# Kernel tuning notes

Measured on AMD Instinct MI355X. Metric: run time of the kernel, lower is better.

## Reference

```python
import jax, jax.numpy as jnp
import numpy as np

D_IN, H1, H2, F1 = 2048, 128, 64, 32


def setup_inputs() -> dict:
    key = jax.random.key(0)
    ks = jax.random.split(key, 13)
    s = lambda *sh: 1.0 / np.sqrt(sh[-1])
    return {
        "x": jax.random.normal(ks[0], (64, 512, D_IN), dtype=jnp.float32),
        "W_ih1": jax.random.uniform(ks[1], (H1, D_IN), jnp.float32, -s(H1), s(H1)),
        "W_hh1": jax.random.uniform(ks[2], (H1, H1), jnp.float32, -s(H1), s(H1)),
        "b_ih1": jax.random.uniform(ks[3], (H1,), jnp.float32, -s(H1), s(H1)),
        "b_hh1": jax.random.uniform(ks[4], (H1,), jnp.float32, -s(H1), s(H1)),
        "W_ih2": jax.random.uniform(ks[5], (H2, H1), jnp.float32, -s(H2), s(H2)),
        "W_hh2": jax.random.uniform(ks[6], (H2, H2), jnp.float32, -s(H2), s(H2)),
        "b_ih2": jax.random.uniform(ks[7], (H2,), jnp.float32, -s(H2), s(H2)),
        "b_hh2": jax.random.uniform(ks[8], (H2,), jnp.float32, -s(H2), s(H2)),
        "W_fc1": jax.random.uniform(ks[9], (F1, H2), jnp.float32, -s(F1), s(F1)),
        "b_fc1": jax.random.uniform(ks[10], (F1,), jnp.float32, -s(F1), s(F1)),
        "W_fc2": jax.random.uniform(ks[11], (1, F1), jnp.float32, -s(1), s(1)),
        "b_fc2": jax.random.uniform(ks[12], (1,), jnp.float32, -s(1), s(1)),
    }


def _rnn(x, W_ih, W_hh, b_ih, b_hh):
    # x: [B, T, D] -> outputs [B, T, H] (tanh RNN, h0 = 0)
    B = x.shape[0]
    H = W_hh.shape[0]
    # precompute the input projection once (big GEMM, outside the scan)
    xp = jnp.einsum('btd,hd->bth', x, W_ih) + b_ih  # [B, T, H]
    xp_t = jnp.swapaxes(xp, 0, 1)  # [T, B, H]

    def step(h, xpt):
        h_new = jnp.tanh(xpt + h @ W_hh.T + b_hh)
        return h_new, h_new

    h0 = jnp.zeros((B, H), dtype=x.dtype)
    _, ys = jax.lax.scan(step, h0, xp_t)  # ys: [T, B, H]
    return jnp.swapaxes(ys, 0, 1)


def reference(x, W_ih1, W_hh1, b_ih1, b_hh1, W_ih2, W_hh2, b_ih2, b_hh2,
              W_fc1, b_fc1, W_fc2, b_fc2):
    out1 = _rnn(x, W_ih1, W_hh1, b_ih1, b_hh1)      # [B, T, 128]
    # dropout is identity in eval mode
    out2 = _rnn(out1, W_ih2, W_hh2, b_ih2, b_hh2)   # [B, T, 64]
    h_last = out2[:, -1, :]                          # [B, 64]
    h = jax.nn.relu(h_last @ W_fc1.T + b_fc1)        # [B, 32]
    return h @ W_fc2.T + b_fc2                       # [B, 1]
```

## Files before the change

kernel.cpp:

```cpp
#include <hip/hip_runtime.h>

#define TT   512
#define DIN  2048
#define NH1  128
#define NH2  64
#define NB   64

typedef __attribute__((ext_vector_type(8))) __bf16 bf16x8;
typedef __attribute__((ext_vector_type(4))) float f32x4;
typedef __attribute__((ext_vector_type(2))) float f32x2;

__device__ __forceinline__ float tanh_fast(float x) {
    x = fminf(fmaxf(x, -15.0f), 15.0f);
    float e = __expf(2.0f * x);
    return (e - 1.0f) / (e + 1.0f);
}

__device__ __forceinline__ float rlane(float v, int l) {
    return __int_as_float(__builtin_amdgcn_readlane(__float_as_int(v), l));
}

__device__ __forceinline__ void pkfma(f32x2& acc, f32x2 w, f32x2 h) {
    asm("v_pk_fma_f32 %0, %1, %2, %0" : "+v"(acc) : "v"(w), "v"(h));
}

#define BAR() asm volatile("s_waitcnt lgkmcnt(0)\n\ts_barrier" ::: "memory")

__global__ __launch_bounds__(256, 1) void xp1_gemm(const float* __restrict__ x,
                                                   const float* __restrict__ W,
                                                   const float* __restrict__ bih1,
                                                   const float* __restrict__ bhh1,
                                                   float* __restrict__ xp1) {
    __shared__ __align__(16) __bf16 wl[2][NH1][40];

    const int tid  = threadIdx.x;
    const int lane = tid & 63;
    const int wv   = tid >> 6;
    const int quad = lane >> 4;
    const int l16  = lane & 15;
    const int m0   = blockIdx.x * 128 + wv * 32;

    const int wr = tid >> 1;
    const int wk = (tid & 1) * 16;

    float bias[8];
#pragma unroll
    for (int nt = 0; nt < 8; ++nt)
        bias[nt] = bih1[nt * 16 + l16] + bhh1[nt * 16 + l16];

    f32x4 acc[2][8];
#pragma unroll
    for (int ms = 0; ms < 2; ++ms)
#pragma unroll
        for (int nt = 0; nt < 8; ++nt)
            acc[ms][nt] = (f32x4){0.f, 0.f, 0.f, 0.f};

    const float* xr0 = x + (size_t)(m0 + l16) * DIN + quad * 8;
    const float* xr1 = x + (size_t)(m0 + 16 + l16) * DIN + quad * 8;
    const float* wp  = W + (size_t)wr * DIN + wk;

    float4 xa0 = *(const float4*)(xr0);
    float4 xb0 = *(const float4*)(xr0 + 4);
    float4 xa1 = *(const float4*)(xr1);
    float4 xb1 = *(const float4*)(xr1 + 4);
    float4 w0  = *(const float4*)(wp);
    float4 w1  = *(const float4*)(wp + 4);
    float4 w2  = *(const float4*)(wp + 8);
    float4 w3  = *(const float4*)(wp + 12);

    for (int kc = 0; kc < DIN; kc += 32) {
        {
            float wf[16] = {w0.x, w0.y, w0.z, w0.w, w1.x, w1.y, w1.z, w1.w,
                            w2.x, w2.y, w2.z, w2.w, w3.x, w3.y, w3.z, w3.w};
            bf16x8 hv0, lv0, hv1, lv1;
#pragma unroll
            for (int j = 0; j < 8; ++j) {
                __bf16 h = (__bf16)wf[j];
                hv0[j] = h;
                lv0[j] = (__bf16)(wf[j] - (float)h);
            }
#pragma unroll
            for (int j = 0; j < 8; ++j) {
                __bf16 h = (__bf16)wf[8 + j];
                hv1[j] = h;
                lv1[j] = (__bf16)(wf[8 + j] - (float)h);
            }
            *(bf16x8*)&wl[0][wr][wk]     = hv0;
            *(bf16x8*)&wl[0][wr][wk + 8] = hv1;
            *(bf16x8*)&wl[1][wr][wk]     = lv0;
            *(bf16x8*)&wl[1][wr][wk + 8] = lv1;
        }
        BAR();

        bf16x8 ah0, al0, ah1, al1;
        {
            float f0[8] = {xa0.x, xa0.y, xa0.z, xa0.w, xb0.x, xb0.y, xb0.z, xb0.w};
            float f1[8] = {xa1.x, xa1.y, xa1.z, xa1.w, xb1.x, xb1.y, xb1.z, xb1.w};
#pragma unroll
            for (int j = 0; j < 8; ++j) {
                __bf16 h0 = (__bf16)f0[j];
                ah0[j] = h0;
                al0[j] = (__bf16)(f0[j] - (float)h0);
                __bf16 h1 = (__bf16)f1[j];
                ah1[j] = h1;
                al1[j] = (__bf16)(f1[j] - (float)h1);
            }
        }

        if (kc + 32 < DIN) {
            xa0 = *(const float4*)(xr0 + kc + 32);
            xb0 = *(const float4*)(xr0 + kc + 36);
            xa1 = *(const float4*)(xr1 + kc + 32);
            xb1 = *(const float4*)(xr1 + kc + 36);
            w0  = *(const float4*)(wp + kc + 32);
            w1  = *(const float4*)(wp + kc + 36);
            w2  = *(const float4*)(wp + kc + 40);
            w3  = *(const float4*)(wp + kc + 44);
        }

#pragma unroll
        for (int nt = 0; nt < 8; ++nt) {
            bf16x8 bh = *(bf16x8*)&wl[0][nt * 16 + l16][quad * 8];
            bf16x8 bl = *(bf16x8*)&wl[1][nt * 16 + l16][quad * 8];
            acc[0][nt] = __builtin_amdgcn_mfma_f32_16x16x32_bf16(ah0, bh, acc[0][nt], 0, 0, 0);
            acc[0][nt] = __builtin_amdgcn_mfma_f32_16x16x32_bf16(al0, bh, acc[0][nt], 0, 0, 0);
            acc[0][nt] = __builtin_amdgcn_mfma_f32_16x16x32_bf16(ah0, bl, acc[0][nt], 0, 0, 0);
            acc[1][nt] = __builtin_amdgcn_mfma_f32_16x16x32_bf16(ah1, bh, acc[1][nt], 0, 0, 0);
            acc[1][nt] = __builtin_amdgcn_mfma_f32_16x16x32_bf16(al1, bh, acc[1][nt], 0, 0, 0);
            acc[1][nt] = __builtin_amdgcn_mfma_f32_16x16x32_bf16(ah1, bl, acc[1][nt], 0, 0, 0);
        }
        BAR();
    }

#pragma unroll
    for (int ms = 0; ms < 2; ++ms) {
        const int mb = m0 + ms * 16 + quad * 4;
#pragma unroll
        for (int nt = 0; nt < 8; ++nt) {
#pragma unroll
            for (int r = 0; r < 4; ++r)
                xp1[(size_t)(mb + r) * NH1 + nt * 16 + l16] = acc[ms][nt][r] + bias[nt];
        }
    }
}

__global__ __launch_bounds__(256, 1) void rnn_scan(
        const float* __restrict__ xp1,  const float* __restrict__ Whh1,
        const float* __restrict__ Wih2, const float* __restrict__ Whh2,
        const float* __restrict__ bih2, const float* __restrict__ bhh2,
        const float* __restrict__ Wfc1, const float* __restrict__ bfc1,
        const float* __restrict__ Wfc2, const float* __restrict__ bfc2,
        float* __restrict__ out) {
    __shared__ __align__(16) float h1buf[2][NH1];
    __shared__ __align__(16) float xp2buf[2][NH2];
    __shared__ __align__(16) float h2buf[2][NH2];

    const int tid  = threadIdx.x;
    const int lane = tid & 63;
    const int wv   = tid >> 6;
    const int b    = blockIdx.x;

    f32x2 w2[64];
    float b2 = 0.0f;

    if (wv <= 1) {
        const int row = wv * 64 + lane;
        const float4* src = (const float4*)(Whh1 + (size_t)row * NH1);
#pragma unroll
        for (int i = 0; i < 32; ++i) {
            float4 v = src[i];
            w2[2 * i]     = (f32x2){v.x, v.y};
            w2[2 * i + 1] = (f32x2){v.z, v.w};
        }
    } else if (wv == 2) {
        const float4* src = (const float4*)(Wih2 + (size_t)lane * NH1);
#pragma unroll
        for (int i = 0; i < 32; ++i) {
            float4 v = src[i];
            w2[2 * i]     = (f32x2){v.x, v.y};
            w2[2 * i + 1] = (f32x2){v.z, v.w};
        }
        b2 = bih2[lane] + bhh2[lane];
    } else {
        const float4* src = (const float4*)(Whh2 + (size_t)lane * NH2);
#pragma unroll
        for (int i = 0; i < 16; ++i) {
            float4 v = src[i];
            w2[2 * i]     = (f32x2){v.x, v.y};
            w2[2 * i + 1] = (f32x2){v.z, v.w};
        }
    }

    if (tid < 128) h1buf[0][tid] = 0.0f;
    if (tid < 64)  { h2buf[0][tid] = 0.0f; h2buf[1][tid] = 0.0f; }

    const int row = wv * 64 + lane;
    const float* xprow = xp1 + ((size_t)b * TT) * NH1 + row;

    float xr[8], xrn[8];
    if (wv <= 1) {
#pragma unroll
        for (int j = 0; j < 8; ++j) xr[j] = xprow[(size_t)j * NH1];
    }

    __syncthreads();

    for (int g = 0; g < 64; ++g) {
        if (wv <= 1 && g < 63) {
            const size_t t0 = (size_t)(g + 1) * 8;
#pragma unroll
            for (int j = 0; j < 8; ++j) xrn[j] = xprow[(t0 + j) * NH1];
        }
#pragma unroll
        for (int j = 0; j < 8; ++j) {
            const int s   = 8 * g + j + 1;
            const int cur = j & 1;
            const int nxt = cur ^ 1;
            if (wv <= 1) {
                f32x2 aA = (f32x2){xr[j], 0.0f};
                f32x2 aB = (f32x2){0.0f, 0.0f};
#pragma unroll
                for (int i = 0; i < 32; ++i) {
                    float4 h4 = *(const float4*)&h1buf[cur][4 * i];
                    pkfma(aA, w2[2 * i],     (f32x2){h4.x, h4.y});
                    pkfma(aB, w2[2 * i + 1], (f32x2){h4.z, h4.w});
                }
                float hv = tanh_fast((aA.x + aA.y) + (aB.x + aB.y));
                h1buf[nxt][row] = hv;
            } else if (wv == 2) {
                if (s >= 2) {
                    f32x2 aA = (f32x2){b2, 0.0f};
                    f32x2 aB = (f32x2){0.0f, 0.0f};
#pragma unroll
                    for (int i = 0; i < 32; ++i) {
                        float4 h4 = *(const float4*)&h1buf[cur][4 * i];
                        pkfma(aA, w2[2 * i],     (f32x2){h4.x, h4.y});
                        pkfma(aB, w2[2 * i + 1], (f32x2){h4.z, h4.w});
                    }
                    xp2buf[j & 1][lane] = (aA.x + aA.y) + (aB.x + aB.y);
                }
            } else {
                if (s >= 3) {
                    float xv = xp2buf[(j + 1) & 1][lane];
                    f32x2 aA = (f32x2){0.0f, 0.0f};
                    f32x2 aB = (f32x2){0.0f, 0.0f};
#pragma unroll
                    for (int i = 0; i < 16; ++i) {
                        float4 h4 = *(const float4*)&h2buf[cur][4 * i];
                        pkfma(aA, w2[2 * i],     (f32x2){h4.x, h4.y});
                        pkfma(aB, w2[2 * i + 1], (f32x2){h4.z, h4.w});
                    }
                    float h2v = tanh_fast(xv + ((aA.x + aA.y) + (aB.x + aB.y)));
                    h2buf[nxt][lane] = h2v;
                }
            }
            BAR();
        }
        if (wv <= 1 && g < 63) {
#pragma unroll
            for (int j = 0; j < 8; ++j) xr[j] = xrn[j];
        }
    }

    {
        if (wv == 2) {
            f32x2 aA = (f32x2){b2, 0.0f};
            f32x2 aB = (f32x2){0.0f, 0.0f};
#pragma unroll
            for (int i = 0; i < 32; ++i) {
                float4 h4 = *(const float4*)&h1buf[0][4 * i];
                pkfma(aA, w2[2 * i],     (f32x2){h4.x, h4.y});
                pkfma(aB, w2[2 * i + 1], (f32x2){h4.z, h4.w});
            }
            xp2buf[0][lane] = (aA.x + aA.y) + (aB.x + aB.y);
        } else if (wv == 3) {
            float xv = xp2buf[1][lane];
            f32x2 aA = (f32x2){0.0f, 0.0f};
            f32x2 aB = (f32x2){0.0f, 0.0f};
#pragma unroll
            for (int i = 0; i < 16; ++i) {
                float4 h4 = *(const float4*)&h2buf[0][4 * i];
                pkfma(aA, w2[2 * i],     (f32x2){h4.x, h4.y});
                pkfma(aB, w2[2 * i + 1], (f32x2){h4.z, h4.w});
            }
            float h2v = tanh_fast(xv + ((aA.x + aA.y) + (aB.x + aB.y)));
            h2buf[1][lane] = h2v;
        }
        BAR();
    }
    if (wv == 3) {
        float xv = xp2buf[0][lane];
        f32x2 aA = (f32x2){0.0f, 0.0f};
        f32x2 aB = (f32x2){0.0f, 0.0f};
#pragma unroll
        for (int i = 0; i < 16; ++i) {
            float4 h4 = *(const float4*)&h2buf[1][4 * i];
            pkfma(aA, w2[2 * i],     (f32x2){h4.x, h4.y});
            pkfma(aB, w2[2 * i + 1], (f32x2){h4.z, h4.w});
        }
        float h2last = tanh_fast(xv + ((aA.x + aA.y) + (aB.x + aB.y)));

        float wfc[64];
        const int fr = lane & 31;
        const float4* fsrc = (const float4*)(Wfc1 + (size_t)fr * NH2);
#pragma unroll
        for (int i = 0; i < 16; ++i) {
            float4 v = fsrc[i];
            wfc[4*i+0] = v.x; wfc[4*i+1] = v.y;
            wfc[4*i+2] = v.z; wfc[4*i+3] = v.w;
        }
        float a = (lane < 32) ? bfc1[lane] : 0.0f;
#pragma unroll
        for (int k = 0; k < 64; ++k)
            a = fmaf(wfc[k], rlane(h2last, k), a);
        float v = (lane < 32) ? fmaxf(a, 0.0f) * Wfc2[lane] : 0.0f;
#pragma unroll
        for (int off = 16; off > 0; off >>= 1) v += __shfl_down(v, off);
        if (lane == 0) out[b] = v + bfc2[0];
    }
}

extern "C" void kernel_launch(void* const* d_in, const int* in_sizes, int n_in,
                              void* d_out, int out_size, void* d_ws, size_t ws_size,
                              hipStream_t stream) {
    const float* x     = (const float*)d_in[0];
    const float* Wih1  = (const float*)d_in[1];
    const float* Whh1  = (const float*)d_in[2];
    const float* bih1  = (const float*)d_in[3];
    const float* bhh1  = (const float*)d_in[4];
    const float* Wih2  = (const float*)d_in[5];
    const float* Whh2  = (const float*)d_in[6];
    const float* bih2  = (const float*)d_in[7];
    const float* bhh2  = (const float*)d_in[8];
    const float* Wfc1  = (const float*)d_in[9];
    const float* bfc1  = (const float*)d_in[10];
    const float* Wfc2  = (const float*)d_in[11];
    const float* bfc2  = (const float*)d_in[12];
    float* outp = (float*)d_out;

    float* xp1 = (float*)d_ws;

    xp1_gemm<<<dim3((NB * TT) / 128), dim3(256), 0, stream>>>(x, Wih1, bih1, bhh1, xp1);
    rnn_scan<<<dim3(NB), dim3(256), 0, stream>>>(xp1, Whh1, Wih2, Whh2, bih2, bhh2,
                                                 Wfc1, bfc1, Wfc2, bfc2, outp);
}
```

Before: 717.0 us.

## Batch 16 sequences per block and run recurrence on MFMA with split-bf16

The recurrent scan now processes 16 sequences per workgroup and computes the hidden-state matvecs as 16x16x32 bf16 MFMAs. Weights and hidden states are split into hi/lo bf16 pairs, and three MFMAs per tile approximate fp32 precision. Hidden states live in XOR-swizzled LDS buffers. All four waves now share layer-1, the layer-2 input projection and the layer-2 recurrence instead of having dedicated roles. This reduces the grid from 64 blocks to 4, trading parallelism across CUs for more work per serial step, and the split-bf16 scheme carries some precision risk.

```diff
diff --git a/kernel.cpp b/kernel.cpp
--- a/kernel.cpp
+++ b/kernel.cpp
@@ -7,21 +7,13 @@
 #define NB   64
 
 typedef __attribute__((ext_vector_type(8))) __bf16 bf16x8;
+typedef __attribute__((ext_vector_type(4))) __bf16 bf16x4;
 typedef __attribute__((ext_vector_type(4))) float f32x4;
-typedef __attribute__((ext_vector_type(2))) float f32x2;
 
 __device__ __forceinline__ float tanh_fast(float x) {
     x = fminf(fmaxf(x, -15.0f), 15.0f);
     float e = __expf(2.0f * x);
     return (e - 1.0f) / (e + 1.0f);
-}
-
-__device__ __forceinline__ float rlane(float v, int l) {
-    return __int_as_float(__builtin_amdgcn_readlane(__float_as_int(v), l));
-}
-
-__device__ __forceinline__ void pkfma(f32x2& acc, f32x2 w, f32x2 h) {
-    asm("v_pk_fma_f32 %0, %1, %2, %0" : "+v"(acc) : "v"(w), "v"(h));
 }
 
 #define BAR() asm volatile("s_waitcnt lgkmcnt(0)\n\ts_barrier" ::: "memory")
@@ -144,6 +136,118 @@
     }
 }
 
+
+__device__ __forceinline__ f32x4 mfma3(bf16x8 ah, bf16x8 al, bf16x8 bh, bf16x8 bl, f32x4 c) {
+    c = __builtin_amdgcn_mfma_f32_16x16x32_bf16(ah, bh, c, 0, 0, 0);
+    c = __builtin_amdgcn_mfma_f32_16x16x32_bf16(al, bh, c, 0, 0, 0);
+    c = __builtin_amdgcn_mfma_f32_16x16x32_bf16(ah, bl, c, 0, 0, 0);
+    return c;
+}
+
+__device__ __forceinline__ void tanh_split4(const f32x4& a, bf16x4& hv, bf16x4& lv) {
+#pragma unroll
+    for (int r = 0; r < 4; ++r) {
+        float t = tanh_fast(a[r]);
+        __bf16 h = (__bf16)t;
+        hv[r] = h;
+        lv[r] = (__bf16)(t - (float)h);
+    }
+}
+
+__device__ __forceinline__ void load_split8(const float* p, bf16x8& hv, bf16x8& lv) {
+    float4 u = *(const float4*)p;
+    float4 v = *(const float4*)(p + 4);
+    float f[8] = {u.x, u.y, u.z, u.w, v.x, v.y, v.z, v.w};
+#pragma unroll
+    for (int j = 0; j < 8; ++j) {
+        __bf16 h = (__bf16)f[j];
+        hv[j] = h;
+        lv[j] = (__bf16)(f[j] - (float)h);
+    }
+}
+
+template <int CUR>
+__device__ __forceinline__ void scan_step(
+        int s, int wv, int q, int l16, int sw, int s0,
+        const float* __restrict__ xp1,
+        __bf16 (&h1hi)[2][16][NH1], __bf16 (&h1lo)[2][16][NH1],
+        __bf16 (&h2hi)[2][16][NH2], __bf16 (&h2lo)[2][16][NH2],
+        const bf16x8 (&a1h)[2][4], const bf16x8 (&a1l)[2][4],
+        const bf16x8 (&a2h)[4],    const bf16x8 (&a2l)[4],
+        const bf16x8 (&a3h)[2],    const bf16x8 (&a3l)[2],
+        const f32x4& b2f, f32x4& xpPrev, f32x4& x0, f32x4& x1) {
+    const int NXT = CUR ^ 1;
+
+    bf16x8 bh1[4], bl1[4];
+    {
+        const char* rbh = (const char*)&h1hi[CUR][l16][0];
+        const char* rbl = (const char*)&h1lo[CUR][l16][0];
+#pragma unroll
+        for (int kt = 0; kt < 4; ++kt) {
+            const int boff = (kt * 64 + q * 16) ^ sw;
+            bh1[kt] = *(const bf16x8*)(rbh + boff);
+            bl1[kt] = *(const bf16x8*)(rbl + boff);
+        }
+    }
+
+    f32x4 acc0 = x0;
+    f32x4 acc1 = x1;
+#pragma unroll
+    for (int kt = 0; kt < 4; ++kt)
+        acc0 = mfma3(a1h[0][kt], a1l[0][kt], bh1[kt], bl1[kt], acc0);
+#pragma unroll
+    for (int kt = 0; kt < 4; ++kt)
+        acc1 = mfma3(a1h[1][kt], a1l[1][kt], bh1[kt], bl1[kt], acc1);
+
+    bf16x4 hv0, lv0, hv1, lv1;
+    tanh_split4(acc0, hv0, lv0);
+    tanh_split4(acc1, hv1, lv1);
+    {
+        char* wbh = (char*)&h1hi[NXT][l16][0];
+        char* wbl = (char*)&h1lo[NXT][l16][0];
+        const int w0 = ((wv * 32 + q * 4) * 2) ^ sw;
+        const int w1 = ((wv * 32 + 16 + q * 4) * 2) ^ sw;
+        *(bf16x4*)(wbh + w0) = hv0;
+        *(bf16x4*)(wbl + w0) = lv0;
+        *(bf16x4*)(wbh + w1) = hv1;
+        *(bf16x4*)(wbl + w1) = lv1;
+    }
+
+    if (s + 2 <= TT) {
+        const float* p = xp1 + ((size_t)(s0 + l16) * TT + (s + 1)) * NH1 + wv * 32 + q * 4;
+        x0 = *(const f32x4*)p;
+        x1 = *(const f32x4*)(p + 16);
+    }
+
+    f32x4 x2 = b2f;
+#pragma unroll
+    for (int kt = 0; kt < 4; ++kt)
+        x2 = mfma3(a2h[kt], a2l[kt], bh1[kt], bl1[kt], x2);
+
+    if (s >= 3) {
+        bf16x8 bh2[2], bl2[2];
+        const char* r2h = (const char*)&h2hi[CUR][l16][0];
+        const char* r2l = (const char*)&h2lo[CUR][l16][0];
+#pragma unroll
+        for (int kt = 0; kt < 2; ++kt) {
+            const int boff = (kt * 64 + q * 16) ^ sw;
+            bh2[kt] = *(const bf16x8*)(r2h + boff);
+            bl2[kt] = *(const bf16x8*)(r2l + boff);
+        }
+        f32x4 a2 = xpPrev;
+#pragma unroll
+        for (int kt = 0; kt < 2; ++kt)
+            a2 = mfma3(a3h[kt], a3l[kt], bh2[kt], bl2[kt], a2);
+        bf16x4 hv2, lv2;
+        tanh_split4(a2, hv2, lv2);
+        const int w2o = ((wv * 16 + q * 4) * 2) ^ sw;
+        *(bf16x4*)((char*)&h2hi[NXT][l16][0] + w2o) = hv2;
+        *(bf16x4*)((char*)&h2lo[NXT][l16][0] + w2o) = lv2;
+    }
+    xpPrev = x2;
+    BAR();
+}
+
 __global__ __launch_bounds__(256, 1) void rnn_scan(
         const float* __restrict__ xp1,  const float* __restrict__ Whh1,
         const float* __restrict__ Wih2, const float* __restrict__ Whh2,
@@ -151,172 +255,165 @@
         const float* __restrict__ Wfc1, const float* __restrict__ bfc1,
         const float* __restrict__ Wfc2, const float* __restrict__ bfc2,
         float* __restrict__ out) {
-    __shared__ __align__(16) float h1buf[2][NH1];
-    __shared__ __align__(16) float xp2buf[2][NH2];
-    __shared__ __align__(16) float h2buf[2][NH2];
+    __shared__ __align__(16) __bf16 h1hi[2][16][NH1];
+    __shared__ __align__(16) __bf16 h1lo[2][16][NH1];
+    __shared__ __align__(16) __bf16 h2hi[2][16][NH2];
+    __shared__ __align__(16) __bf16 h2lo[2][16][NH2];
+    __shared__ __align__(16) float  h2fin[16][NH2];
 
     const int tid  = threadIdx.x;
     const int lane = tid & 63;
     const int wv   = tid >> 6;
-    const int b    = blockIdx.x;
-
-    f32x2 w2[64];
-    float b2 = 0.0f;
-
-    if (wv <= 1) {
-        const int row = wv * 64 + lane;
-        const float4* src = (const float4*)(Whh1 + (size_t)row * NH1);
-#pragma unroll
-        for (int i = 0; i < 32; ++i) {
-            float4 v = src[i];
-            w2[2 * i]     = (f32x2){v.x, v.y};
-            w2[2 * i + 1] = (f32x2){v.z, v.w};
-        }
-    } else if (wv == 2) {
-        const float4* src = (const float4*)(Wih2 + (size_t)lane * NH1);
-#pragma unroll
-        for (int i = 0; i < 32; ++i) {
-            float4 v = src[i];
-            w2[2 * i]     = (f32x2){v.x, v.y};
-            w2[2 * i + 1] = (f32x2){v.z, v.w};
-        }
-        b2 = bih2[lane] + bhh2[lane];
-    } else {
-        const float4* src = (const float4*)(Whh2 + (size_t)lane * NH2);
-#pragma unroll
-        for (int i = 0; i < 16; ++i) {
-            float4 v = src[i];
-            w2[2 * i]     = (f32x2){v.x, v.y};
-            w2[2 * i + 1] = (f32x2){v.z, v.w};
-        }
-    }
-
-    if (tid < 128) h1buf[0][tid] = 0.0f;
-    if (tid < 64)  { h2buf[0][tid] = 0.0f; h2buf[1][tid] = 0.0f; }
-
-    const int row = wv * 64 + lane;
-    const float* xprow = xp1 + ((size_t)b * TT) * NH1 + row;
-
-    float xr[8], xrn[8];
-    if (wv <= 1) {
-#pragma unroll
-        for (int j = 0; j < 8; ++j) xr[j] = xprow[(size_t)j * NH1];
+    const int q    = lane >> 4;
+    const int l16  = lane & 15;
+    const int sw   = (l16 & 7) << 4;
+    const int s0   = blockIdx.x * 16;
+
+    bf16x8 a1h[2][4], a1l[2][4];
+#pragma unroll
+    for (int mt = 0; mt < 2; ++mt)
+#pragma unroll
+        for (int kt = 0; kt < 4; ++kt)
+            load_split8(Whh1 + (size_t)(wv * 32 + mt * 16 + l16) * NH1 + kt * 32 + q * 8,
+                        a1h[mt][kt], a1l[mt][kt]);
+
+    bf16x8 a2h[4], a2l[4];
+#pragma unroll
+    for (int kt = 0; kt < 4; ++kt)
+        load_split8(Wih2 + (size_t)(wv * 16 + l16) * NH1 + kt * 32 + q * 8,
+                    a2h[kt], a2l[kt]);
+
+    bf16x8 a3h[2], a3l[2];
+#pragma unroll
+    for (int kt = 0; kt < 2; ++kt)
+        load_split8(Whh2 + (size_t)(wv * 16 + l16) * NH2 + kt * 32 + q * 8,
+                    a3h[kt], a3l[kt]);
+
+    f32x4 b2f;
+    {
+        float4 u = *(const float4*)&bih2[wv * 16 + q * 4];
+        float4 v = *(const float4*)&bhh2[wv * 16 + q * 4];
+        b2f = (f32x4){u.x + v.x, u.y + v.y, u.z + v.z, u.w + v.w};
+    }
+
+    {
+        bf16x8 z8;
+#pragma unroll
+        for (int j = 0; j < 8; ++j) z8[j] = (__bf16)0.0f;
+        ((bf16x8*)&h1hi[0][0][0])[tid] = z8;
+        ((bf16x8*)&h1lo[0][0][0])[tid] = z8;
+        if (tid < 128) {
+            ((bf16x8*)&h2hi[0][0][0])[tid] = z8;
+            ((bf16x8*)&h2lo[0][0][0])[tid] = z8;
+        }
+    }
+
+    f32x4 xA0, xA1, xB0, xB1;
+    {
+        const float* p1 = xp1 + ((size_t)(s0 + l16) * TT + 0) * NH1 + wv * 32 + q * 4;
+        const float* p2 = xp1 + ((size_t)(s0 + l16) * TT + 1) * NH1 + wv * 32 + q * 4;
+        xA0 = *(const f32x4*)p1;
+        xA1 = *(const f32x4*)(p1 + 16);
+        xB0 = *(const f32x4*)p2;
+        xB1 = *(const f32x4*)(p2 + 16);
     }
 
     __syncthreads();
 
-    for (int g = 0; g < 64; ++g) {
-        if (wv <= 1 && g < 63) {
-            const size_t t0 = (size_t)(g + 1) * 8;
-#pragma unroll
-            for (int j = 0; j < 8; ++j) xrn[j] = xprow[(t0 + j) * NH1];
-        }
-#pragma unroll
-        for (int j = 0; j < 8; ++j) {
-            const int s   = 8 * g + j + 1;
-            const int cur = j & 1;
-            const int nxt = cur ^ 1;
-            if (wv <= 1) {
-                f32x2 aA = (f32x2){xr[j], 0.0f};
-                f32x2 aB = (f32x2){0.0f, 0.0f};
-#pragma unroll
-                for (int i = 0; i < 32; ++i) {
-                    float4 h4 = *(const float4*)&h1buf[cur][4 * i];
-                    pkfma(aA, w2[2 * i],     (f32x2){h4.x, h4.y});
-                    pkfma(aB, w2[2 * i + 1], (f32x2){h4.z, h4.w});
-                }
-                float hv = tanh_fast((aA.x + aA.y) + (aB.x + aB.y));
-                h1buf[nxt][row] = hv;
-            } else if (wv == 2) {
-                if (s >= 2) {
-                    f32x2 aA = (f32x2){b2, 0.0f};
-                    f32x2 aB = (f32x2){0.0f, 0.0f};
-#pragma unroll
-                    for (int i = 0; i < 32; ++i) {
-                        float4 h4 = *(const float4*)&h1buf[cur][4 * i];
-                        pkfma(aA, w2[2 * i],     (f32x2){h4.x, h4.y});
-                        pkfma(aB, w2[2 * i + 1], (f32x2){h4.z, h4.w});
-                    }
-                    xp2buf[j & 1][lane] = (aA.x + aA.y) + (aB.x + aB.y);
-                }
-            } else {
-                if (s >= 3) {
-                    float xv = xp2buf[(j + 1) & 1][lane];
-                    f32x2 aA = (f32x2){0.0f, 0.0f};
-                    f32x2 aB = (f32x2){0.0f, 0.0f};
-#pragma unroll
-                    for (int i = 0; i < 16; ++i) {
-                        float4 h4 = *(const float4*)&h2buf[cur][4 * i];
-                        pkfma(aA, w2[2 * i],     (f32x2){h4.x, h4.y});
-                        pkfma(aB, w2[2 * i + 1], (f32x2){h4.z, h4.w});
-                    }
-                    float h2v = tanh_fast(xv + ((aA.x + aA.y) + (aB.x + aB.y)));
-                    h2buf[nxt][lane] = h2v;
-                }
+    f32x4 xpPrev = (f32x4){0.f, 0.f, 0.f, 0.f};
+
+    for (int s = 1; s <= TT - 1; s += 2) {
+        scan_step<0>(s,     wv, q, l16, sw, s0, xp1, h1hi, h1lo, h2hi, h2lo,
+                     a1h, a1l, a2h, a2l, a3h, a3l, b2f, xpPrev, xA0, xA1);
+        scan_step<1>(s + 1, wv, q, l16, sw, s0, xp1, h1hi, h1lo, h2hi, h2lo,
+                     a1h, a1l, a2h, a2l, a3h, a3l, b2f, xpPrev, xB0, xB1);
+    }
+
+    {
+        bf16x8 bh1[4], bl1[4];
+        const char* rbh = (const char*)&h1hi[0][l16][0];
+        const char* rbl = (const char*)&h1lo[0][l16][0];
+#pragma unroll
+        for (int kt = 0; kt < 4; ++kt) {
+            const int boff = (kt * 64 + q * 16) ^ sw;
+            bh1[kt] = *(const bf16x8*)(rbh + boff);
+            bl1[kt] = *(const bf16x8*)(rbl + boff);
+        }
+        f32x4 x2 = b2f;
+#pragma unroll
+        for (int kt = 0; kt < 4; ++kt)
+            x2 = mfma3(a2h[kt], a2l[kt], bh1[kt], bl1[kt], x2);
+
+        bf16x8 bh2[2], bl2[2];
+        const char* r2h = (const char*)&h2hi[0][l16][0];
+        const char* r2l = (const char*)&h2lo[0][l16][0];
+#pragma unroll
+        for (int kt = 0; kt < 2; ++kt) {
+            const int boff = (kt * 64 + q * 16) ^ sw;
+            bh2[kt] = *(const bf16x8*)(r2h + boff);
+            bl2[kt] = *(const bf16x8*)(r2l + boff);
+        }
+        f32x4 a2 = xpPrev;
+#pragma unroll
+        for (int kt = 0; kt < 2; ++kt)
+            a2 = mfma3(a3h[kt], a3l[kt], bh2[kt], bl2[kt], a2);
+        bf16x4 hv2, lv2;
+        tanh_split4(a2, hv2, lv2);
+        const int w2o = ((wv * 16 + q * 4) * 2) ^ sw;
+        *(bf16x4*)((char*)&h2hi[1][l16][0] + w2o) = hv2;
+        *(bf16x4*)((char*)&h2lo[1][l16][0] + w2o) = lv2;
+        xpPrev = x2;
+        BAR();
+    }
+
+    {
+        bf16x8 bh2[2], bl2[2];
+        const char* r2h = (const char*)&h2hi[1][l16][0];
+        const char* r2l = (const char*)&h2lo[1][l16][0];
+#pragma unroll
+        for (int kt = 0; kt < 2; ++kt) {
+            const int boff = (kt * 64 + q * 16) ^ sw;
+            bh2[kt] = *(const bf16x8*)(r2h + boff);
+            bl2[kt] = *(const bf16x8*)(r2l + boff);
+        }
+        f32x4 a2 = xpPrev;
+#pragma unroll
+        for (int kt = 0; kt < 2; ++kt)
+            a2 = mfma3(a3h[kt], a3l[kt], bh2[kt], bl2[kt], a2);
+        f32x4 tt;
+#pragma unroll
+        for (int r = 0; r < 4; ++r) tt[r] = tanh_fast(a2[r]);
+        *(f32x4*)&h2fin[l16][wv * 16 + q * 4] = tt;
+        BAR();
+    }
+
+    if (wv == 0) {
+        const int seq = lane & 15;
+        const int c   = lane >> 4;
+        float hreg[NH2];
+#pragma unroll
+        for (int i = 0; i < 16; ++i)
+            *(f32x4*)&hreg[4 * i] = *(const f32x4*)&h2fin[seq][4 * i];
+
+        float accv = 0.0f;
+#pragma unroll
+        for (int i = 0; i < 8; ++i) {
+            const int r = c * 8 + i;
+            float f = bfc1[r];
+            const float* wr = Wfc1 + (size_t)r * NH2;
+#pragma unroll
+            for (int k4 = 0; k4 < 16; ++k4) {
+                float4 wv4 = *(const float4*)(wr + 4 * k4);
+                f = fmaf(wv4.x, hreg[4 * k4 + 0], f);
+                f = fmaf(wv4.y, hreg[4 * k4 + 1], f);
+                f = fmaf(wv4.z, hreg[4 * k4 + 2], f);
+                f = fmaf(wv4.w, hreg[4 * k4 + 3], f);
             }
-            BAR();
-        }
-        if (wv <= 1 && g < 63) {
-#pragma unroll
-            for (int j = 0; j < 8; ++j) xr[j] = xrn[j];
-        }
-    }
-
-    {
-        if (wv == 2) {
-            f32x2 aA = (f32x2){b2, 0.0f};
-            f32x2 aB = (f32x2){0.0f, 0.0f};
-#pragma unroll
-            for (int i = 0; i < 32; ++i) {
-                float4 h4 = *(const float4*)&h1buf[0][4 * i];
-                pkfma(aA, w2[2 * i],     (f32x2){h4.x, h4.y});
-                pkfma(aB, w2[2 * i + 1], (f32x2){h4.z, h4.w});
-            }
-            xp2buf[0][lane] = (aA.x + aA.y) + (aB.x + aB.y);
-        } else if (wv == 3) {
-            float xv = xp2buf[1][lane];
-            f32x2 aA = (f32x2){0.0f, 0.0f};
-            f32x2 aB = (f32x2){0.0f, 0.0f};
-#pragma unroll
-            for (int i = 0; i < 16; ++i) {
-                float4 h4 = *(const float4*)&h2buf[0][4 * i];
-                pkfma(aA, w2[2 * i],     (f32x2){h4.x, h4.y});
-                pkfma(aB, w2[2 * i + 1], (f32x2){h4.z, h4.w});
-            }
-            float h2v = tanh_fast(xv + ((aA.x + aA.y) + (aB.x + aB.y)));
-            h2buf[1][lane] = h2v;
-        }
-        BAR();
-    }
-    if (wv == 3) {
-        float xv = xp2buf[0][lane];
-        f32x2 aA = (f32x2){0.0f, 0.0f};
-        f32x2 aB = (f32x2){0.0f, 0.0f};
-#pragma unroll
-        for (int i = 0; i < 16; ++i) {
-            float4 h4 = *(const float4*)&h2buf[1][4 * i];
-            pkfma(aA, w2[2 * i],     (f32x2){h4.x, h4.y});
-            pkfma(aB, w2[2 * i + 1], (f32x2){h4.z, h4.w});
-        }
-        float h2last = tanh_fast(xv + ((aA.x + aA.y) + (aB.x + aB.y)));
-
-        float wfc[64];
-        const int fr = lane & 31;
-        const float4* fsrc = (const float4*)(Wfc1 + (size_t)fr * NH2);
-#pragma unroll
-        for (int i = 0; i < 16; ++i) {
-            float4 v = fsrc[i];
-            wfc[4*i+0] = v.x; wfc[4*i+1] = v.y;
-            wfc[4*i+2] = v.z; wfc[4*i+3] = v.w;
-        }
-        float a = (lane < 32) ? bfc1[lane] : 0.0f;
-#pragma unroll
-        for (int k = 0; k < 64; ++k)
-            a = fmaf(wfc[k], rlane(h2last, k), a);
-        float v = (lane < 32) ? fmaxf(a, 0.0f) * Wfc2[lane] : 0.0f;
-#pragma unroll
-        for (int off = 16; off > 0; off >>= 1) v += __shfl_down(v, off);
-        if (lane == 0) out[b] = v + bfc2[0];
+            accv += fmaxf(f, 0.0f) * Wfc2[r];
+        }
+        accv += __shfl_down(accv, 32);
+        accv += __shfl_down(accv, 16);
+        if (lane < 16) out[s0 + lane] = accv + bfc2[0];
     }
 }
 
@@ -341,6 +438,6 @@
     float* xp1 = (float*)d_ws;
 
     xp1_gemm<<<dim3((NB * TT) / 128), dim3(256), 0, stream>>>(x, Wih1, bih1, bhh1, xp1);
-    rnn_scan<<<dim3(NB), dim3(256), 0, stream>>>(xp1, Whh1, Wih2, Whh2, bih2, bhh2,
-                                                 Wfc1, bfc1, Wfc2, bfc2, outp);
-}
+    rnn_scan<<<dim3(NB / 16), dim3(256), 0, stream>>>(xp1, Whh1, Wih2, Whh2, bih2, bhh2,
+                                                      Wfc1, bfc1, Wfc2, bfc2, outp);
+}
```

New measurement: 908.9 us. 26.8% more time.
